# Kernel tuning notes

Hardware: AMD Instinct MI355X
Metric: run time of the kernel (lower is better)

Reference implementation:

```python
import jax, jax.numpy as jnp
import numpy as np

D_MODEL = 1024
N_HEADS = 16
HEAD_DIM = D_MODEL // N_HEADS
MAX_POS = 4096
ROPE_BASE = 10000.0
NEG_INF = -1e30


def _rope_cache(max_pos, head_dim, base):
    inv_freq = 1.0 / (base ** (np.arange(0, head_dim, 2, dtype=np.float32) / head_dim))
    t = np.arange(max_pos, dtype=np.float32)[:, None] * inv_freq[None, :]  # [P, D/2]
    cos = np.repeat(np.cos(t), 2, axis=-1)  # [P, D] (repeat_interleave)
    sin = np.repeat(np.sin(t), 2, axis=-1)
    return jnp.asarray(cos), jnp.asarray(sin)

COS_CACHE, SIN_CACHE = _rope_cache(MAX_POS, HEAD_DIM, ROPE_BASE)


def _rotate_half(x):
    # interleaved pairs: (x0,x1,x2,x3,...) -> (-x1,x0,-x3,x2,...)
    x1 = x[..., ::2]
    x2 = x[..., 1::2]
    return jnp.stack((-x2, x1), axis=-1).reshape(x.shape)


def setup_inputs() -> dict:
    key = jax.random.key(0)
    k0, k1, k2 = jax.random.split(key, 3)
    B, S = 4, 1024
    hidden_states = jax.random.normal(k0, (B, S, D_MODEL), dtype=jnp.float32)
    positions = jnp.arange(S, dtype=jnp.int64 if jax.config.jax_enable_x64 else jnp.int32)
    causal_mask = jnp.triu(jnp.ones((S, S), dtype=bool), k=1)  # True above diagonal -> masked
    # learned params (torch nn.Linear weight layout: [out, in], y = x @ W.T)
    Wqkv = jax.random.normal(k1, (3 * D_MODEL, D_MODEL), dtype=jnp.float32) * (D_MODEL ** -0.5)
    Wout = jax.random.normal(k2, (D_MODEL, D_MODEL), dtype=jnp.float32) * (D_MODEL ** -0.5)
    return {"hidden_states": hidden_states, "positions": positions,
            "causal_mask": causal_mask, "Wqkv": Wqkv, "Wout": Wout}


def reference(hidden_states, positions, causal_mask, Wqkv, Wout):
    B, S, D = hidden_states.shape
    qkv = hidden_states @ Wqkv.T                                   # [B,S,3D]
    qkv = qkv.reshape(B, S, 3, N_HEADS, HEAD_DIM)
    qkv = jnp.transpose(qkv, (2, 0, 3, 1, 4))                      # [3,B,H,S,Dh]
    q, k, v = qkv[0], qkv[1], qkv[2]
    # RoPE
    pos = jnp.clip(positions, 0, MAX_POS - 1)
    if pos.ndim == 1:
        pos = pos[None, :]
    cos = COS_CACHE[pos][:, None, :, :].astype(q.dtype)            # [B,1,S,Dh]
    sin = SIN_CACHE[pos][:, None, :, :].astype(q.dtype)
    q = q * cos + _rotate_half(q) * sin
    k = k * cos + _rotate_half(k) * sin
    # SDPA with causal bias (F.scaled_dot_product_attention default scaling)
    scale = HEAD_DIM ** -0.5
    scores = jnp.einsum('bhqd,bhkd->bhqk', q, k) * scale           # [B,H,S,S]
    scores = jnp.where(causal_mask[None, None, :, :], NEG_INF, scores)
    probs = jax.nn.softmax(scores, axis=-1)
    attn = jnp.einsum('bhqk,bhkd->bhqd', probs, v)                 # [B,H,S,Dh]
    attn = jnp.transpose(attn, (0, 2, 1, 3)).reshape(B, S, D)
    return attn @ Wout.T
```

## Files before the change

### kernel.cpp

```cpp
#include <hip/hip_runtime.h>

typedef __attribute__((ext_vector_type(8))) short short8;
typedef __attribute__((ext_vector_type(4))) float f32x4;

#define MFMA(a, b, c) __builtin_amdgcn_mfma_f32_16x16x32_bf16((a), (b), (c), 0, 0, 0)

#define S_LEN 1024
#define DM 1024
#define NHEADS 16
#define HD 64
#define NBH 64
#define MAXPOS 4096

__device__ __forceinline__ ushort f2bf(float f) {
    unsigned u = __builtin_bit_cast(unsigned, f);
    u += 0x7fffu + ((u >> 16) & 1u);
    return (ushort)(u >> 16);
}
__device__ __forceinline__ float bf2f(ushort h) {
    return __builtin_bit_cast(float, (unsigned)h << 16);
}

__device__ __forceinline__ void gload16(const ushort* g, ushort* l) {
    __builtin_amdgcn_global_load_lds(
        (const __attribute__((address_space(1))) unsigned int*)g,
        (__attribute__((address_space(3))) unsigned int*)l, 16, 0, 0);
}

__global__ __launch_bounds__(256) void k_cvt3(const float4* __restrict__ hs,
                                              const float4* __restrict__ wqkv,
                                              const float4* __restrict__ wout,
                                              ushort4* __restrict__ hsB,
                                              ushort4* __restrict__ wqkvB,
                                              ushort4* __restrict__ woutB,
                                              float* __restrict__ tab) {
    int id = blockIdx.x * 256 + threadIdx.x;
    if (id < 2097152) {
        const float4* src;
        ushort4* dst;
        int off;
        if (id < 1048576)      { src = hs;   dst = hsB;   off = id; }
        else if (id < 1835008) { src = wqkv; dst = wqkvB; off = id - 1048576; }
        else                   { src = wout; dst = woutB; off = id - 1835008; }
        float4 v = src[off];
        ushort4 o;
        o.x = f2bf(v.x); o.y = f2bf(v.y); o.z = f2bf(v.z); o.w = f2bf(v.w);
        dst[off] = o;
    } else {
        int t = id - 2097152;
        int p = t >> 5, i = t & 31;
        float inv = powf(10000.f, -(float)(2 * i) / 64.f);
        float th = (float)p * inv;
        float s, c;
        sincosf(th, &s, &c);
        tab[2 * t] = c;
        tab[2 * t + 1] = s;
    }
}

template <int MODE>
__global__ __launch_bounds__(512, 6) void k_gemm(
    const ushort* __restrict__ A, const ushort* __restrict__ BT,
    float* __restrict__ Cf,
    const int* __restrict__ pos, const float* __restrict__ tab,
    ushort* __restrict__ Qh, ushort* __restrict__ Kh, ushort* __restrict__ Vt,
    int M, int N, int K, int nbx) {
    __shared__ __align__(16) ushort SH[3 * 8192];
    const int tid = threadIdx.x;
    const int lane = tid & 63, wave = tid >> 6;
    const int wr = wave >> 2, wc = wave & 3;
    const int l15 = lane & 15, lhi = lane >> 4;
    const int nby = gridDim.x / nbx;
    const int xcd = blockIdx.x & 7, idx = blockIdx.x >> 3;
    const int Creg = nbx >> 1, Rreg = nby >> 2;
    const int by = (xcd >> 1) * Rreg + idx / Creg;
    const int bx = (xcd & 1) * Creg + idx % Creg;
    const int m0 = by << 7, n0 = bx << 7;

    const int srow = tid >> 2;
    const int scol = (((tid & 3) ^ (srow & 3) ^ ((srow >> 2) & 3)) << 3);
    const int fcol = ((lhi ^ ((l15 & 3) ^ ((l15 >> 2) & 3)))) << 3;

    f32x4 acc[4][2];
#pragma unroll
    for (int i = 0; i < 4; ++i)
#pragma unroll
        for (int j = 0; j < 2; ++j) acc[i][j] = 0;

#define STAGE(bs, kb)                                                           \
    do {                                                                        \
        ushort* bb = SH + (bs) * 8192;                                          \
        gload16(&A[(size_t)(m0 + srow) * K + (kb) + scol], bb + tid * 8);       \
        gload16(&BT[(size_t)(n0 + srow) * K + (kb) + scol],                     \
                bb + 4096 + tid * 8);                                           \
    } while (0)

    const int nk = K >> 5;
    STAGE(0, 0);
    STAGE(1, 32);
    int bi = 0;
    for (int t = 0; t < nk; ++t) {
        if (t + 1 < nk) {
            asm volatile("s_waitcnt vmcnt(2)" ::: "memory");
        } else {
            asm volatile("s_waitcnt vmcnt(0)" ::: "memory");
        }
        __builtin_amdgcn_s_barrier();
        __builtin_amdgcn_sched_barrier(0);
        if (t + 2 < nk) {
            int bs = bi + 2;
            if (bs >= 3) bs -= 3;
            STAGE(bs, (t + 2) << 5);
        }
        const ushort* bufA = SH + bi * 8192;
        const ushort* bufB = bufA + 4096;
        short8 a[4], b[2];
#pragma unroll
        for (int fm = 0; fm < 4; ++fm)
            a[fm] = *(const short8*)&bufA[(wr * 64 + fm * 16 + l15) * 32 + fcol];
#pragma unroll
        for (int fn = 0; fn < 2; ++fn)
            b[fn] = *(const short8*)&bufB[(wc * 32 + fn * 16 + l15) * 32 + fcol];
#pragma unroll
        for (int fm = 0; fm < 4; ++fm)
#pragma unroll
            for (int fn = 0; fn < 2; ++fn)
                acc[fm][fn] = MFMA(a[fm], b[fn], acc[fm][fn]);
        bi = (bi == 2) ? 0 : bi + 1;
    }
#undef STAGE
    __syncthreads();

    if (MODE == 0) {
#pragma unroll
        for (int fm = 0; fm < 4; ++fm)
#pragma unroll
            for (int fn = 0; fn < 2; ++fn)
#pragma unroll
                for (int i = 0; i < 4; ++i) {
                    int row = m0 + wr * 64 + fm * 16 + lhi * 4 + i;
                    int col = n0 + wc * 32 + fn * 16 + l15;
                    Cf[(size_t)row * N + col] = acc[fm][fn][i];
                }
    } else {
        const int sec = n0 >> 10;
        if (sec < 2) {
            ushort* dstb = sec == 0 ? Qh : Kh;
            const float qs = sec == 0 ? 0.125f : 1.0f;
#pragma unroll
            for (int fm = 0; fm < 4; ++fm)
#pragma unroll
                for (int i = 0; i < 4; ++i) {
                    const int row = m0 + wr * 64 + fm * 16 + lhi * 4 + i;
                    const int b = row >> 10, s = row & 1023;
                    int p = pos[s];
                    p = p < 0 ? 0 : (p > MAXPOS - 1 ? MAXPOS - 1 : p);
#pragma unroll
                    for (int fn = 0; fn < 2; ++fn) {
                        const int col = n0 + wc * 32 + fn * 16 + l15;
                        const int cw = col & 1023;
                        const int h = cw >> 6, d = cw & 63;
                        const float c  = tab[((size_t)p * 32 + (d >> 1)) * 2];
                        const float sn = tab[((size_t)p * 32 + (d >> 1)) * 2 + 1];
                        const float v = acc[fm][fn][i];
                        const float pr = __shfl_xor(v, 1);
                        const float o = (d & 1) ? (v * c + pr * sn) : (v * c - pr * sn);
                        dstb[((size_t)((b * 16 + h) * 1024 + s)) * 64 + d] = f2bf(o * qs);
                    }
                }
        } else {
            ushort (*T)[132] = (ushort(*)[132]) & SH[0];
#pragma unroll
            for (int fm = 0; fm < 4; ++fm)
#pragma unroll
                for (int fn = 0; fn < 2; ++fn)
#pragma unroll
                    for (int i = 0; i < 4; ++i)
                        T[wr * 64 + fm * 16 + lhi * 4 + i][wc * 32 + fn * 16 + l15] =
                            f2bf(acc[fm][fn][i]);
            __syncthreads();
            const int b = m0 >> 10, s0 = m0 & 1023;
            const int dd = tid & 127, grp = tid >> 7;
            const int hv = ((n0 & 1023) >> 6) + (dd >> 6);
            const int d = dd & 63;
            ushort* dst = Vt + ((size_t)(b * 16 + hv) * 64 + d) * S_LEN + s0;
#pragma unroll
            for (int j = 0; j < 4; ++j) {
                const int ch = grp * 4 + j;
                __align__(16) ushort tmp[8];
#pragma unroll
                for (int e = 0; e < 8; ++e) tmp[e] = T[ch * 8 + e][dd];
                *(uint4*)&dst[ch * 8] = *(uint4*)tmp;
            }
        }
    }
}

__global__ __launch_bounds__(256, 3) void k_attn(const ushort* __restrict__ Qh,
                                                 const ushort* __restrict__ Kh,
                                                 const ushort* __restrict__ Vt,
                                                 ushort* __restrict__ attnB) {
    __shared__ __align__(16) ushort Ks[2][64][64];
    __shared__ __align__(16) ushort Vs[2][64][64];
    __shared__ __align__(16) ushort P[4][16][72];
    const int bh = blockIdx.x;
    const int g  = blockIdx.y;
    const int gA = g, gB = 15 - g;
    const int nkb = gB + 1;
    const int tid = threadIdx.x;
    const int wave = tid >> 6, lane = tid & 63;
    const int l15 = lane & 15, lhi = lane >> 4;
    const int b = bh >> 4, h = bh & 15;
    const ushort* Qp = Qh + (size_t)bh * S_LEN * 64;
    const ushort* Kp = Kh + (size_t)bh * S_LEN * 64;
    const ushort* Vp = Vt + (size_t)bh * 64 * S_LEN;
    const int qbA = (gA << 6) + (wave << 4);
    const int qbB = (gB << 6) + (wave << 4);
    const int qrowbA = qbA + lhi * 4;
    const int qrowbB = qbB + lhi * 4;

    const int U0 = tid, U1 = tid + 256;
    const int r0 = U0 >> 3, o0 = ((U0 & 7) ^ (r0 & 7)) << 3;
    const int r1 = U1 >> 3, o1 = ((U1 & 7) ^ (r1 & 7)) << 3;
    ushort* KsF = &Ks[0][0][0];
    ushort* VsF = &Vs[0][0][0];

    short8 aQA0 = *(const short8*)&Qp[(size_t)(qbA + l15) * 64 + lhi * 8];
    short8 aQA1 = *(const short8*)&Qp[(size_t)(qbA + l15) * 64 + 32 + lhi * 8];
    short8 aQB0 = *(const short8*)&Qp[(size_t)(qbB + l15) * 64 + lhi * 8];
    short8 aQB1 = *(const short8*)&Qp[(size_t)(qbB + l15) * 64 + 32 + lhi * 8];

    short8 ones;
#pragma unroll
    for (int j = 0; j < 8; ++j) ones[j] = (short)0x3F80;

    f32x4 OA0{}, OA1{}, OA2{}, OA3{}, ssumA{};
    f32x4 OB0{}, OB1{}, OB2{}, OB3{}, ssumB{};

    gload16(&Kp[(size_t)r0 * 64 + o0], KsF + U0 * 8);
    gload16(&Kp[(size_t)r1 * 64 + o1], KsF + U1 * 8);
    gload16(&Vp[(size_t)r0 * S_LEN + o0], VsF + U0 * 8);
    gload16(&Vp[(size_t)r1 * S_LEN + o1], VsF + U1 * 8);
    __syncthreads();

#define LDSK(s, kk) (*(const short8*)(KsF + (cur << 12) + ((((s) << 4) + l15) << 6) + \
                                      ((((kk) * 4 + lhi) ^ (l15 & 7)) << 3)))
#define LDSV(n, kk) (*(const short8*)(VsF + (cur << 12) + ((((n) << 4) + l15) << 6) + \
                                      ((((kk) * 4 + lhi) ^ (l15 & 7)) << 3)))
#define EXPST(SV, SUB)                                                         \
    _Pragma("unroll") for (int i = 0; i < 4; ++i) {                            \
        P[wave][lhi * 4 + i][(SUB) * 16 + l15] = f2bf(__expf(SV[i] - 8.f));    \
    }
#define EXPSTM(SV, SUB, QROWB)                                                 \
    _Pragma("unroll") for (int i = 0; i < 4; ++i) {                            \
        float v = SV[i];                                                       \
        if (k0 + (SUB) * 16 + l15 > (QROWB) + i) v = -1e30f;                   \
        P[wave][lhi * 4 + i][(SUB) * 16 + l15] = f2bf(__expf(v - 8.f));        \
    }

    int cur = 0;
    for (int kb = 0; kb < nkb; ++kb) {
        const int k0 = kb << 6;
        if (kb + 1 < nkb) {
            const int kn = k0 + 64;
            const int bo = (cur ^ 1) << 12;
            gload16(&Kp[(size_t)(kn + r0) * 64 + o0], KsF + bo + U0 * 8);
            gload16(&Kp[(size_t)(kn + r1) * 64 + o1], KsF + bo + U1 * 8);
            gload16(&Vp[(size_t)r0 * S_LEN + kn + o0], VsF + bo + U0 * 8);
            gload16(&Vp[(size_t)r1 * S_LEN + kn + o1], VsF + bo + U1 * 8);
        }

        if (kb <= gA) {
            __builtin_amdgcn_s_setprio(1);
            f32x4 s0{}, s1{}, s2{}, s3{};
            s0 = MFMA(aQA0, LDSK(0, 0), s0); s0 = MFMA(aQA1, LDSK(0, 1), s0);
            s1 = MFMA(aQA0, LDSK(1, 0), s1); s1 = MFMA(aQA1, LDSK(1, 1), s1);
            s2 = MFMA(aQA0, LDSK(2, 0), s2); s2 = MFMA(aQA1, LDSK(2, 1), s2);
            s3 = MFMA(aQA0, LDSK(3, 0), s3); s3 = MFMA(aQA1, LDSK(3, 1), s3);
            __builtin_amdgcn_s_setprio(0);
            if (kb == gA) {
                EXPSTM(s0, 0, qrowbA) EXPSTM(s1, 1, qrowbA)
                EXPSTM(s2, 2, qrowbA) EXPSTM(s3, 3, qrowbA)
            } else {
                EXPST(s0, 0) EXPST(s1, 1) EXPST(s2, 2) EXPST(s3, 3)
            }
            short8 aP0 = *(const short8*)&P[wave][l15][lhi * 8];
            short8 aP1 = *(const short8*)&P[wave][l15][32 + lhi * 8];
            __builtin_amdgcn_s_setprio(1);
            ssumA = MFMA(aP0, ones, ssumA); ssumA = MFMA(aP1, ones, ssumA);
            OA0 = MFMA(aP0, LDSV(0, 0), OA0); OA0 = MFMA(aP1, LDSV(0, 1), OA0);
            OA1 = MFMA(aP0, LDSV(1, 0), OA1); OA1 = MFMA(aP1, LDSV(1, 1), OA1);
            OA2 = MFMA(aP0, LDSV(2, 0), OA2); OA2 = MFMA(aP1, LDSV(2, 1), OA2);
            OA3 = MFMA(aP0, LDSV(3, 0), OA3); OA3 = MFMA(aP1, LDSV(3, 1), OA3);
            __builtin_amdgcn_s_setprio(0);
        }

        {
            __builtin_amdgcn_s_setprio(1);
            f32x4 s0{}, s1{}, s2{}, s3{};
            s0 = MFMA(aQB0, LDSK(0, 0), s0); s0 = MFMA(aQB1, LDSK(0, 1), s0);
            s1 = MFMA(aQB0, LDSK(1, 0), s1); s1 = MFMA(aQB1, LDSK(1, 1), s1);
            s2 = MFMA(aQB0, LDSK(2, 0), s2); s2 = MFMA(aQB1, LDSK(2, 1), s2);
            s3 = MFMA(aQB0, LDSK(3, 0), s3); s3 = MFMA(aQB1, LDSK(3, 1), s3);
            __builtin_amdgcn_s_setprio(0);
            if (kb == gB) {
                EXPSTM(s0, 0, qrowbB) EXPSTM(s1, 1, qrowbB)
                EXPSTM(s2, 2, qrowbB) EXPSTM(s3, 3, qrowbB)
            } else {
                EXPST(s0, 0) EXPST(s1, 1) EXPST(s2, 2) EXPST(s3, 3)
            }
            short8 aP0 = *(const short8*)&P[wave][l15][lhi * 8];
            short8 aP1 = *(const short8*)&P[wave][l15][32 + lhi * 8];
            __builtin_amdgcn_s_setprio(1);
            ssumB = MFMA(aP0, ones, ssumB); ssumB = MFMA(aP1, ones, ssumB);
            OB0 = MFMA(aP0, LDSV(0, 0), OB0); OB0 = MFMA(aP1, LDSV(0, 1), OB0);
            OB1 = MFMA(aP0, LDSV(1, 0), OB1); OB1 = MFMA(aP1, LDSV(1, 1), OB1);
            OB2 = MFMA(aP0, LDSV(2, 0), OB2); OB2 = MFMA(aP1, LDSV(2, 1), OB2);
            OB3 = MFMA(aP0, LDSV(3, 0), OB3); OB3 = MFMA(aP1, LDSV(3, 1), OB3);
            __builtin_amdgcn_s_setprio(0);
        }

        __syncthreads();
        cur ^= 1;
    }
#undef LDSK
#undef LDSV
#undef EXPST
#undef EXPSTM

#define WOUT(OV, N, QB, INV)                                                   \
    _Pragma("unroll") for (int i = 0; i < 4; ++i) {                            \
        int row = (QB) + lhi * 4 + i;                                          \
        attnB[((size_t)(b * S_LEN + row)) * DM + h * 64 + (N) * 16 + l15] =    \
            f2bf(OV[i] * INV[i]);                                              \
    }
    {
        f32x4 invA, invB;
#pragma unroll
        for (int i = 0; i < 4; ++i) {
            invA[i] = 1.f / ssumA[i];
            invB[i] = 1.f / ssumB[i];
        }
        WOUT(OA0, 0, qbA, invA) WOUT(OA1, 1, qbA, invA)
        WOUT(OA2, 2, qbA, invA) WOUT(OA3, 3, qbA, invA)
        WOUT(OB0, 0, qbB, invB) WOUT(OB1, 1, qbB, invB)
        WOUT(OB2, 2, qbB, invB) WOUT(OB3, 3, qbB, invB)
    }
#undef WOUT
}

extern "C" void kernel_launch(void* const* d_in, const int* in_sizes, int n_in,
                              void* d_out, int out_size, void* d_ws, size_t ws_size,
                              hipStream_t stream) {
    (void)in_sizes; (void)n_in; (void)out_size; (void)ws_size;
    const float* hs   = (const float*)d_in[0];
    const int*   pos  = (const int*)d_in[1];
    const float* Wqkv = (const float*)d_in[3];
    const float* Wout = (const float*)d_in[4];
    float* out = (float*)d_out;

    char* ws = (char*)d_ws;
    size_t off = 0;
    ushort* hsB   = (ushort*)(ws + off); off += (size_t)4096 * 1024 * 2;
    ushort* WqkvB = (ushort*)(ws + off); off += (size_t)3072 * 1024 * 2;
    ushort* WoutB = (ushort*)(ws + off); off += (size_t)1024 * 1024 * 2;
    ushort* Qh    = (ushort*)(ws + off); off += (size_t)NBH * 1024 * 64 * 2;
    ushort* Kh    = (ushort*)(ws + off); off += (size_t)NBH * 1024 * 64 * 2;
    ushort* Vt    = (ushort*)(ws + off); off += (size_t)NBH * 64 * 1024 * 2;
    ushort* attnB = (ushort*)(ws + off); off += (size_t)4096 * 1024 * 2;
    float*  tab   = (float*)(ws + off);  off += (size_t)4096 * 32 * 2 * 4;

    k_cvt3<<<8704, 256, 0, stream>>>((const float4*)hs, (const float4*)Wqkv,
                                     (const float4*)Wout, (ushort4*)hsB,
                                     (ushort4*)WqkvB, (ushort4*)WoutB, tab);

    k_gemm<1><<<768, 512, 0, stream>>>(hsB, WqkvB, nullptr, pos, tab,
                                       Qh, Kh, Vt, 4096, 3072, 1024, 24);

    k_attn<<<dim3(64, 8), 256, 0, stream>>>(Qh, Kh, Vt, attnB);

    k_gemm<0><<<256, 512, 0, stream>>>(attnB, WoutB, out, nullptr, nullptr,
                                       nullptr, nullptr, nullptr, 4096, 1024, 1024, 8);
}
```

Measured before the change: 93.39 us.

## Widen attention KV tiles to 128 keys with swizzled P buffer

The attention kernel now stages 128-key K/V tiles per iteration instead of 64, which halves the number of loop iterations and block barriers. The P scratch buffer is widened to 128 columns with an XOR swizzle to avoid LDS bank conflicts. Launch bounds drop from 3 to 2 blocks per SM to fit the doubled LDS use. On the diagonal tile, up to half of the 128-key block is masked work. Lower occupancy and more registers per thread could reduce latency hiding.

```diff
diff --git a/kernel.cpp b/kernel.cpp
--- a/kernel.cpp
+++ b/kernel.cpp
@@ -196,17 +196,18 @@
     }
 }
 
-__global__ __launch_bounds__(256, 3) void k_attn(const ushort* __restrict__ Qh,
+__global__ __launch_bounds__(256, 2) void k_attn(const ushort* __restrict__ Qh,
                                                  const ushort* __restrict__ Kh,
                                                  const ushort* __restrict__ Vt,
                                                  ushort* __restrict__ attnB) {
-    __shared__ __align__(16) ushort Ks[2][64][64];
-    __shared__ __align__(16) ushort Vs[2][64][64];
-    __shared__ __align__(16) ushort P[4][16][72];
+    __shared__ __align__(16) ushort Ks[2][128][64];
+    __shared__ __align__(16) ushort Vs[2][64][128];
+    __shared__ __align__(16) ushort P[4][16][128];
     const int bh = blockIdx.x;
     const int g  = blockIdx.y;
     const int gA = g, gB = 15 - g;
-    const int nkb = gB + 1;
+    const int nkbA = (gA + 2) >> 1;
+    const int nkbB = (gB + 2) >> 1;
     const int tid = threadIdx.x;
     const int wave = tid >> 6, lane = tid & 63;
     const int l15 = lane & 15, lhi = lane >> 4;
@@ -219,11 +220,9 @@
     const int qrowbA = qbA + lhi * 4;
     const int qrowbB = qbB + lhi * 4;
 
-    const int U0 = tid, U1 = tid + 256;
-    const int r0 = U0 >> 3, o0 = ((U0 & 7) ^ (r0 & 7)) << 3;
-    const int r1 = U1 >> 3, o1 = ((U1 & 7) ^ (r1 & 7)) << 3;
     ushort* KsF = &Ks[0][0][0];
     ushort* VsF = &Vs[0][0][0];
+    ushort* Pw  = &P[wave][0][0];
 
     short8 aQA0 = *(const short8*)&Qp[(size_t)(qbA + l15) * 64 + lhi * 8];
     short8 aQA1 = *(const short8*)&Qp[(size_t)(qbA + l15) * 64 + 32 + lhi * 8];
@@ -237,96 +236,89 @@
     f32x4 OA0{}, OA1{}, OA2{}, OA3{}, ssumA{};
     f32x4 OB0{}, OB1{}, OB2{}, OB3{}, ssumB{};
 
-    gload16(&Kp[(size_t)r0 * 64 + o0], KsF + U0 * 8);
-    gload16(&Kp[(size_t)r1 * 64 + o1], KsF + U1 * 8);
-    gload16(&Vp[(size_t)r0 * S_LEN + o0], VsF + U0 * 8);
-    gload16(&Vp[(size_t)r1 * S_LEN + o1], VsF + U1 * 8);
+#define STAGEKV(bo, k0s)                                                        \
+    do {                                                                        \
+        _Pragma("unroll") for (int k = 0; k < 4; ++k) {                         \
+            const int u = tid + k * 256;                                        \
+            const int r = u >> 3, c = u & 7;                                    \
+            gload16(&Kp[(size_t)((k0s) + r) * 64 + ((c ^ (r & 7)) << 3)],       \
+                    KsF + (bo) + u * 8);                                        \
+        }                                                                       \
+        _Pragma("unroll") for (int k = 0; k < 4; ++k) {                         \
+            const int u = tid + k * 256;                                        \
+            const int r = u >> 4, c = u & 15;                                   \
+            const int cs = c ^ (r & 7);                                         \
+            gload16(&Vp[(size_t)r * S_LEN + (k0s) + cs * 8], VsF + (bo) + u * 8); \
+        }                                                                       \
+    } while (0)
+
+#define LDSK(s, kk) (*(const short8*)(KsF + (cur << 13) + ((((s) << 4) + l15) << 6) + \
+                                      (((((kk) << 2) + lhi) ^ (l15 & 7)) << 3)))
+#define LDSV(n, kk) (*(const short8*)(VsF + (cur << 13) + ((((n) << 4) + l15) << 7) + \
+                                      (((((kk) << 2) + lhi) ^ (l15 & 7)) << 3)))
+
+    STAGEKV(0, 0);
     __syncthreads();
 
-#define LDSK(s, kk) (*(const short8*)(KsF + (cur << 12) + ((((s) << 4) + l15) << 6) + \
-                                      ((((kk) * 4 + lhi) ^ (l15 & 7)) << 3)))
-#define LDSV(n, kk) (*(const short8*)(VsF + (cur << 12) + ((((n) << 4) + l15) << 6) + \
-                                      ((((kk) * 4 + lhi) ^ (l15 & 7)) << 3)))
-#define EXPST(SV, SUB)                                                         \
-    _Pragma("unroll") for (int i = 0; i < 4; ++i) {                            \
-        P[wave][lhi * 4 + i][(SUB) * 16 + l15] = f2bf(__expf(SV[i] - 8.f));    \
-    }
-#define EXPSTM(SV, SUB, QROWB)                                                 \
-    _Pragma("unroll") for (int i = 0; i < 4; ++i) {                            \
-        float v = SV[i];                                                       \
-        if (k0 + (SUB) * 16 + l15 > (QROWB) + i) v = -1e30f;                   \
-        P[wave][lhi * 4 + i][(SUB) * 16 + l15] = f2bf(__expf(v - 8.f));        \
-    }
-
     int cur = 0;
-    for (int kb = 0; kb < nkb; ++kb) {
-        const int k0 = kb << 6;
-        if (kb + 1 < nkb) {
-            const int kn = k0 + 64;
-            const int bo = (cur ^ 1) << 12;
-            gload16(&Kp[(size_t)(kn + r0) * 64 + o0], KsF + bo + U0 * 8);
-            gload16(&Kp[(size_t)(kn + r1) * 64 + o1], KsF + bo + U1 * 8);
-            gload16(&Vp[(size_t)r0 * S_LEN + kn + o0], VsF + bo + U0 * 8);
-            gload16(&Vp[(size_t)r1 * S_LEN + kn + o1], VsF + bo + U1 * 8);
-        }
-
-        if (kb <= gA) {
-            __builtin_amdgcn_s_setprio(1);
-            f32x4 s0{}, s1{}, s2{}, s3{};
-            s0 = MFMA(aQA0, LDSK(0, 0), s0); s0 = MFMA(aQA1, LDSK(0, 1), s0);
-            s1 = MFMA(aQA0, LDSK(1, 0), s1); s1 = MFMA(aQA1, LDSK(1, 1), s1);
-            s2 = MFMA(aQA0, LDSK(2, 0), s2); s2 = MFMA(aQA1, LDSK(2, 1), s2);
-            s3 = MFMA(aQA0, LDSK(3, 0), s3); s3 = MFMA(aQA1, LDSK(3, 1), s3);
-            __builtin_amdgcn_s_setprio(0);
-            if (kb == gA) {
-                EXPSTM(s0, 0, qrowbA) EXPSTM(s1, 1, qrowbA)
-                EXPSTM(s2, 2, qrowbA) EXPSTM(s3, 3, qrowbA)
-            } else {
-                EXPST(s0, 0) EXPST(s1, 1) EXPST(s2, 2) EXPST(s3, 3)
-            }
-            short8 aP0 = *(const short8*)&P[wave][l15][lhi * 8];
-            short8 aP1 = *(const short8*)&P[wave][l15][32 + lhi * 8];
-            __builtin_amdgcn_s_setprio(1);
-            ssumA = MFMA(aP0, ones, ssumA); ssumA = MFMA(aP1, ones, ssumA);
-            OA0 = MFMA(aP0, LDSV(0, 0), OA0); OA0 = MFMA(aP1, LDSV(0, 1), OA0);
-            OA1 = MFMA(aP0, LDSV(1, 0), OA1); OA1 = MFMA(aP1, LDSV(1, 1), OA1);
-            OA2 = MFMA(aP0, LDSV(2, 0), OA2); OA2 = MFMA(aP1, LDSV(2, 1), OA2);
-            OA3 = MFMA(aP0, LDSV(3, 0), OA3); OA3 = MFMA(aP1, LDSV(3, 1), OA3);
-            __builtin_amdgcn_s_setprio(0);
-        }
-
-        {
-            __builtin_amdgcn_s_setprio(1);
-            f32x4 s0{}, s1{}, s2{}, s3{};
-            s0 = MFMA(aQB0, LDSK(0, 0), s0); s0 = MFMA(aQB1, LDSK(0, 1), s0);
-            s1 = MFMA(aQB0, LDSK(1, 0), s1); s1 = MFMA(aQB1, LDSK(1, 1), s1);
-            s2 = MFMA(aQB0, LDSK(2, 0), s2); s2 = MFMA(aQB1, LDSK(2, 1), s2);
-            s3 = MFMA(aQB0, LDSK(3, 0), s3); s3 = MFMA(aQB1, LDSK(3, 1), s3);
-            __builtin_amdgcn_s_setprio(0);
-            if (kb == gB) {
-                EXPSTM(s0, 0, qrowbB) EXPSTM(s1, 1, qrowbB)
-                EXPSTM(s2, 2, qrowbB) EXPSTM(s3, 3, qrowbB)
-            } else {
-                EXPST(s0, 0) EXPST(s1, 1) EXPST(s2, 2) EXPST(s3, 3)
-            }
-            short8 aP0 = *(const short8*)&P[wave][l15][lhi * 8];
-            short8 aP1 = *(const short8*)&P[wave][l15][32 + lhi * 8];
-            __builtin_amdgcn_s_setprio(1);
-            ssumB = MFMA(aP0, ones, ssumB); ssumB = MFMA(aP1, ones, ssumB);
-            OB0 = MFMA(aP0, LDSV(0, 0), OB0); OB0 = MFMA(aP1, LDSV(0, 1), OB0);
-            OB1 = MFMA(aP0, LDSV(1, 0), OB1); OB1 = MFMA(aP1, LDSV(1, 1), OB1);
-            OB2 = MFMA(aP0, LDSV(2, 0), OB2); OB2 = MFMA(aP1, LDSV(2, 1), OB2);
-            OB3 = MFMA(aP0, LDSV(3, 0), OB3); OB3 = MFMA(aP1, LDSV(3, 1), OB3);
-            __builtin_amdgcn_s_setprio(0);
-        }
+    for (int kb = 0; kb < nkbB; ++kb) {
+        const int k0 = kb << 7;
+        if (kb + 1 < nkbB) STAGEKV((cur ^ 1) << 13, k0 + 128);
+
+#define TILE_WORK(AQ0, AQ1, QROWB, NKB, O0, O1, O2, O3, SSUM)                   \
+    if (kb < (NKB)) {                                                           \
+        f32x4 sc[8];                                                            \
+        __builtin_amdgcn_s_setprio(1);                                          \
+        _Pragma("unroll") for (int s = 0; s < 8; ++s) {                         \
+            sc[s] = f32x4{0.f, 0.f, 0.f, 0.f};                                  \
+            sc[s] = MFMA(AQ0, LDSK(s, 0), sc[s]);                               \
+            sc[s] = MFMA(AQ1, LDSK(s, 1), sc[s]);                               \
+        }                                                                       \
+        __builtin_amdgcn_s_setprio(0);                                          \
+        if (kb == (NKB) - 1) {                                                  \
+            _Pragma("unroll") for (int s = 0; s < 8; ++s)                       \
+                _Pragma("unroll") for (int i = 0; i < 4; ++i) {                 \
+                    float v = sc[s][i];                                         \
+                    if (k0 + s * 16 + l15 > (QROWB) + i) v = -1e30f;            \
+                    const int row = lhi * 4 + i;                                \
+                    Pw[row * 128 +                                              \
+                       (((s * 2 + (l15 >> 3)) ^ (row & 7)) << 3) + (l15 & 7)] = \
+                        f2bf(__expf(v - 8.f));                                  \
+                }                                                               \
+        } else {                                                                \
+            _Pragma("unroll") for (int s = 0; s < 8; ++s)                       \
+                _Pragma("unroll") for (int i = 0; i < 4; ++i) {                 \
+                    const int row = lhi * 4 + i;                                \
+                    Pw[row * 128 +                                              \
+                       (((s * 2 + (l15 >> 3)) ^ (row & 7)) << 3) + (l15 & 7)] = \
+                        f2bf(__expf(sc[s][i] - 8.f));                           \
+                }                                                               \
+        }                                                                       \
+        short8 aP[4];                                                           \
+        _Pragma("unroll") for (int kk = 0; kk < 4; ++kk)                        \
+            aP[kk] = *(const short8*)&Pw[l15 * 128 +                            \
+                                         ((((kk << 2) + lhi) ^ (l15 & 7)) << 3)]; \
+        __builtin_amdgcn_s_setprio(1);                                          \
+        _Pragma("unroll") for (int kk = 0; kk < 4; ++kk) {                      \
+            SSUM = MFMA(aP[kk], ones, SSUM);                                    \
+            O0 = MFMA(aP[kk], LDSV(0, kk), O0);                                 \
+            O1 = MFMA(aP[kk], LDSV(1, kk), O1);                                 \
+            O2 = MFMA(aP[kk], LDSV(2, kk), O2);                                 \
+            O3 = MFMA(aP[kk], LDSV(3, kk), O3);                                 \
+        }                                                                       \
+        __builtin_amdgcn_s_setprio(0);                                          \
+    }
+
+        TILE_WORK(aQA0, aQA1, qrowbA, nkbA, OA0, OA1, OA2, OA3, ssumA)
+        TILE_WORK(aQB0, aQB1, qrowbB, nkbB, OB0, OB1, OB2, OB3, ssumB)
+#undef TILE_WORK
 
         __syncthreads();
         cur ^= 1;
     }
 #undef LDSK
 #undef LDSV
-#undef EXPST
-#undef EXPSTM
+#undef STAGEKV
 
 #define WOUT(OV, N, QB, INV)                                                   \
     _Pragma("unroll") for (int i = 0; i < 4; ++i) {                            \
```

Result: faster. 90.46 us, median of 4 (-3.1%).
